# Kernel tuning notes

Hardware: AMD Instinct MI355X
Metric: run time of the kernel (lower is better)

The kernel has to match this reference:

```python
import jax, jax.numpy as jnp
import numpy as np

B, T, D, H = 4, 2048, 1024, 16
DK, DV, K, I = 48, 96, 4, 3072
EPS = 1e-5


def rmsnorm(x, w, eps=EPS):
    return x * jax.lax.rsqrt(jnp.mean(x * x, -1, keepdims=True) + eps) * w


def l2norm(x, eps=1e-6):
    return x * jax.lax.rsqrt(jnp.sum(x * x, -1, keepdims=True) + eps)


def causal_conv(x, w):
    # x: [B,T,C], w: [C,K]; causal depthwise conv (torch cross-correlation semantics)
    k = w.shape[1]
    xp = jnp.pad(x, ((0, 0), (k - 1, 0), (0, 0))).transpose(0, 2, 1)  # [B,C,T+K-1]
    y = jax.lax.conv_general_dilated(xp, w[:, None, :], (1,), 'VALID',
                                     feature_group_count=w.shape[0])
    return y.transpose(0, 2, 1)


def gated_delta_rule(q, k, v, g, beta):
    # q,k: [B,T,H,DK]  v: [B,T,H,DV]  g,beta: [B,T,H]
    scale = q.shape[-1] ** -0.5
    qT = jnp.moveaxis(q, 1, 0) * scale
    kT = jnp.moveaxis(k, 1, 0)
    vT = jnp.moveaxis(v, 1, 0)
    gT = jnp.moveaxis(g, 1, 0)
    bT = jnp.moveaxis(beta, 1, 0)
    S0 = jnp.zeros((q.shape[0], q.shape[2], q.shape[3], v.shape[3]), q.dtype)

    def step(S, inp):
        q_t, k_t, v_t, g_t, b_t = inp
        S = S * jnp.exp(g_t)[..., None, None]                      # gated decay
        v_new = (v_t - jnp.einsum('bhk,bhkv->bhv', k_t, S)) * b_t[..., None]
        S = S + k_t[..., None] * v_new[..., None, :]               # delta-rule update
        o_t = jnp.einsum('bhk,bhkv->bhv', q_t, S)
        return S, o_t

    _, o = jax.lax.scan(step, S0, (qT, kT, vT, gT, bT))
    return jnp.moveaxis(o, 0, 1)


def setup_inputs() -> dict:
    key = jax.random.key(0)
    ks = jax.random.split(key, 20)
    s = 0.02
    return {
        'hidden_states': jax.random.normal(ks[0], (B, T, D), jnp.float32),
        'norm1_w': jnp.ones((D,), jnp.float32),
        'q_w': jax.random.normal(ks[1], (D, H * DK), jnp.float32) * s,
        'k_w': jax.random.normal(ks[2], (D, H * DK), jnp.float32) * s,
        'v_w': jax.random.normal(ks[3], (D, H * DV), jnp.float32) * s,
        'conv_q_w': jax.random.normal(ks[4], (H * DK, K), jnp.float32) * 0.2,
        'conv_k_w': jax.random.normal(ks[5], (H * DK, K), jnp.float32) * 0.2,
        'conv_v_w': jax.random.normal(ks[6], (H * DV, K), jnp.float32) * 0.2,
        'b_w': jax.random.normal(ks[7], (D, H), jnp.float32) * s,
        'a_w': jax.random.normal(ks[8], (D, H), jnp.float32) * s,
        'A_log': jnp.log(jax.random.uniform(ks[9], (H,), jnp.float32, 1.0, 16.0)),
        'dt_bias': jax.random.normal(ks[10], (H,), jnp.float32) * 0.5,
        'g_w': jax.random.normal(ks[11], (D, H * DV), jnp.float32) * s,
        'o_norm_w': jnp.ones((DV,), jnp.float32),
        'o_w': jax.random.normal(ks[12], (H * DV, D), jnp.float32) * s,
        'norm2_w': jnp.ones((D,), jnp.float32),
        'gate_w': jax.random.normal(ks[13], (D, I), jnp.float32) * s,
        'up_w': jax.random.normal(ks[14], (D, I), jnp.float32) * s,
        'down_w': jax.random.normal(ks[15], (I, D), jnp.float32) * s,
    }


def reference(hidden_states, norm1_w, q_w, k_w, v_w, conv_q_w, conv_k_w, conv_v_w,
              b_w, a_w, A_log, dt_bias, g_w, o_norm_w, o_w, norm2_w,
              gate_w, up_w, down_w):
    x = hidden_states
    h = rmsnorm(x, norm1_w)
    # --- GatedDeltaNet mixer ---
    q = jax.nn.silu(causal_conv(h @ q_w, conv_q_w)).reshape(B, T, H, DK)
    k = jax.nn.silu(causal_conv(h @ k_w, conv_k_w)).reshape(B, T, H, DK)
    v = jax.nn.silu(causal_conv(h @ v_w, conv_v_w)).reshape(B, T, H, DV)
    q, k = l2norm(q), l2norm(k)
    beta = jax.nn.sigmoid(h @ b_w)                                  # [B,T,H]
    g = -jnp.exp(A_log) * jax.nn.softplus(h @ a_w + dt_bias)        # [B,T,H] mamba gate
    o = gated_delta_rule(q, k, v, g, beta)                          # [B,T,H,DV]
    gate = (h @ g_w).reshape(B, T, H, DV)
    o = rmsnorm(o, o_norm_w) * (gate * jax.nn.sigmoid(gate))        # fused gated RMSNorm
    x = x + o.reshape(B, T, H * DV) @ o_w
    # --- SwiGLU MLP ---
    h2 = rmsnorm(x, norm2_w)
    x = x + (jax.nn.silu(h2 @ gate_w) * (h2 @ up_w)) @ down_w
    return x
```

## Files before the change

kernel.cpp:

```cpp
#include <hip/hip_runtime.h>
#include <hip/hip_bf16.h>
#include <math.h>

constexpr int Bn = 4, Tn = 2048, Dn = 1024, Hn = 16, DKn = 48, DVn = 96, In = 3072;
constexpr int BT = Bn * Tn;
constexpr int HDK = Hn * DKn;
constexpr int HDV = Hn * DVn;
constexpr int QKVC = 2 * HDK + HDV;
constexpr int CC = 64;
constexpr int NC = Tn / CC;

using bf16 = __hip_bfloat16;
typedef __attribute__((ext_vector_type(8))) short bf16x8;
typedef __attribute__((ext_vector_type(4))) float f32x4;

constexpr size_t WO_HBF   = 0;
constexpr size_t WO_QKVR  = 16777216;
constexpr size_t WO_OSC   = 16777216;
constexpr size_t WO_ATTN  = 41943040;
constexpr size_t WO_ACT   = 16777216;
constexpr size_t WO_A     = 16777216;
constexpr size_t WO_B     = 26214400;
constexpr size_t WO_ST    = 45088768;
constexpr size_t WO_QKVC  = 67108864;
constexpr size_t WO_GATE  = 117440512;
constexpr size_t WO_X1    = 142606336;
constexpr size_t WO_BA    = 176160768;
constexpr size_t WO_GC    = 177209344;
constexpr size_t WO_T     = 177733632;
constexpr size_t WO_UV    = 194510848;
constexpr size_t WO_WB    = 219676672;
constexpr size_t WB_QKVT = 0;
constexpr size_t WB_GT   = 3145728;
constexpr size_t WB_OT   = 4718592;
constexpr size_t WB_GATET= 6291456;
constexpr size_t WB_UPT  = 9437184;
constexpr size_t WB_DOWNT= 12582912;
constexpr size_t WB_ABT  = 15728640;

__device__ __forceinline__ float sigmoidf_(float x) { return 1.f / (1.f + __expf(-x)); }
__device__ __forceinline__ float siluf(float x) { return x * sigmoidf_(x); }

__device__ __forceinline__ void glds16(const void* g, void* l) {
  __builtin_amdgcn_global_load_lds((const __attribute__((address_space(1))) void*)g,
                                   (__attribute__((address_space(3))) void*)l, 16, 0, 0);
}

__device__ __forceinline__ f32x4 mfma16(bf16x8 a, bf16x8 b, f32x4 c) {
  return __builtin_amdgcn_mfma_f32_16x16x32_bf16(a, b, c, 0, 0, 0);
}

__device__ __forceinline__ bf16x8 scale8(bf16x8 a, float s) {
  bf16x8 r;
#pragma unroll
  for (int e = 0; e < 8; e++) {
    float f = __bfloat162float(__ushort_as_bfloat16((unsigned short)a[e])) * s;
    r[e] = (short)__bfloat16_as_ushort(__float2bfloat16(f));
  }
  return r;
}

__device__ __forceinline__ float b2f(short u) {
  return __bfloat162float(__ushort_as_bfloat16((unsigned short)u));
}
__device__ __forceinline__ short f2b(float f) {
  return (short)__bfloat16_as_ushort(__float2bfloat16(f));
}

struct TcastArgs {
  const float* src[10];
  bf16* dst[10];
  int R[10], C[10], gxw[10], t0[10];
};

__global__ void tcast_all(TcastArgs a) {
  __shared__ float t[32][33];
  int bid = blockIdx.x;
  int i = 0;
#pragma unroll
  for (int k = 1; k < 10; k++) if (bid >= a.t0[k]) i = k;
  int lt = bid - a.t0[i];
  int gxw = a.gxw[i];
  int bx = lt % gxw, by = lt / gxw;
  const float* in = a.src[i];
  bf16* out = a.dst[i];
  int R = a.R[i], C = a.C[i];
  int tx = threadIdx.x, ty = threadIdx.y;
  int c0 = bx * 32, r0 = by * 32;
#pragma unroll
  for (int j = 0; j < 4; j++) {
    int r = ty + j * 8;
    float v = (c0 + tx < C) ? in[(size_t)(r0 + r) * C + c0 + tx] : 0.f;
    t[r][tx] = v;
  }
  __syncthreads();
#pragma unroll
  for (int j = 0; j < 4; j++) {
    int cc = ty + j * 8;
    if (c0 + cc < C) out[(size_t)(c0 + cc) * R + r0 + tx] = __float2bfloat16(t[tx][cc]);
  }
}

__global__ void rmsnorm_bf_k(const float* __restrict__ x, const float* __restrict__ w,
                             bf16* __restrict__ y) {
  int row = blockIdx.x;
  const float4* xr = (const float4*)(x + (size_t)row * Dn);
  int tid = threadIdx.x;
  float4 v = xr[tid];
  float ss = v.x * v.x + v.y * v.y + v.z * v.z + v.w * v.w;
  for (int m = 32; m >= 1; m >>= 1) ss += __shfl_xor(ss, m, 64);
  __shared__ float wsum[4];
  if ((tid & 63) == 0) wsum[tid >> 6] = ss;
  __syncthreads();
  ss = wsum[0] + wsum[1] + wsum[2] + wsum[3];
  float rs = rsqrtf(ss * (1.f / Dn) + 1e-5f);
  float4 wv = ((const float4*)w)[tid];
  bf16* yr = y + (size_t)row * Dn + tid * 4;
  yr[0] = __float2bfloat16(v.x * rs * wv.x);
  yr[1] = __float2bfloat16(v.y * rs * wv.y);
  yr[2] = __float2bfloat16(v.z * rs * wv.z);
  yr[3] = __float2bfloat16(v.w * rs * wv.w);
}

#define AS256(bi) (lds + (bi) * 8192)
#define BS256(bi) (lds + 32768 + (bi) * 8192)
#define STAGE256(bi, k0) do { \
    glds16(gA0 + (k0), AS256(bi) + w * 512); \
    glds16(gA1 + (k0), AS256(bi) + 4096 + w * 512); \
    glds16(gB0 + (k0), BS256(bi) + w * 512); \
    glds16(gB1 + (k0), BS256(bi) + 4096 + w * 512); \
  } while (0)

__global__ __launch_bounds__(512, 2) void gemm256(
    const bf16* __restrict__ A, const bf16* __restrict__ Bt,
    bf16* __restrict__ C0, bf16* __restrict__ C1,
    int gx, int N, int K, int mode) {
  __shared__ bf16 lds[65536];
  int nb = gx * 32;
  int q8 = nb >> 3;
  int bid = blockIdx.x;
  int sw = (bid & 7) * q8 + (bid >> 3);
  int by = sw & 31, bx = sw >> 5;
  int bm = by * 256, bn = bx * 256;
  int tid = threadIdx.x;
  int lane = tid & 63, w = tid >> 6;
  int l15 = lane & 15, lq = lane >> 4;
  int wr = w >> 2, wc = w & 3;
  int arow0 = tid >> 2;
  int srcq = (tid & 3) ^ ((arow0 >> 1) & 3);
  const bf16* gA0 = A + (size_t)(bm + arow0) * K + srcq * 8;
  const bf16* gA1 = A + (size_t)(bm + 128 + arow0) * K + srcq * 8;
  const bf16* gB0 = Bt + (size_t)(bn + arow0) * K + srcq * 8;
  const bf16* gB1 = Bt + (size_t)(bn + 128 + arow0) * K + srcq * 8;
  int slot = lq ^ ((l15 >> 1) & 3);
  f32x4 acc[8][4];
#pragma unroll
  for (int m = 0; m < 8; m++)
#pragma unroll
    for (int n = 0; n < 4; n++) acc[m][n] = (f32x4){0.f, 0.f, 0.f, 0.f};
  int NT = K >> 5;
  STAGE256(0, 0);
  STAGE256(1, 32);
  STAGE256(2, 64);
  for (int t = 0; t < NT; ++t) {
    int b = t & 3;
    if (t <= NT - 3)      { asm volatile("s_waitcnt vmcnt(8)" ::: "memory"); }
    else if (t == NT - 2) { asm volatile("s_waitcnt vmcnt(4)" ::: "memory"); }
    else                  { asm volatile("s_waitcnt vmcnt(0)" ::: "memory"); }
    __builtin_amdgcn_s_barrier();
    bf16x8 af[8], bfr[4];
#pragma unroll
    for (int m = 0; m < 8; m++)
      af[m] = *(const bf16x8*)(AS256(b) + (wr * 128 + m * 16 + l15) * 32 + slot * 8);
#pragma unroll
    for (int n = 0; n < 4; n++)
      bfr[n] = *(const bf16x8*)(BS256(b) + (wc * 64 + n * 16 + l15) * 32 + slot * 8);
    __builtin_amdgcn_s_setprio(1);
#pragma unroll
    for (int m = 0; m < 8; m++)
#pragma unroll
      for (int n = 0; n < 4; n++)
        acc[m][n] = mfma16(af[m], bfr[n], acc[m][n]);
    __builtin_amdgcn_s_setprio(0);
    if (t + 3 < NT) STAGE256((t + 3) & 3, (t + 3) * 32);
  }
  __syncthreads();
  bf16* dst; int ldc, bnl; bool doSilu;
  if (mode == 10) {
    if (bn < 3072) { dst = C0; ldc = 3072; bnl = bn; doSilu = false; }
    else           { dst = C1; ldc = 1536; bnl = bn - 3072; doSilu = false; }
  } else {
    if (bn < 3072) { dst = C0; ldc = 3072; bnl = bn; doSilu = true; }
    else           { dst = C1; ldc = 3072; bnl = bn - 3072; doSilu = false; }
  }
  bf16* cw = lds + w * 8192;
#pragma unroll
  for (int m = 0; m < 8; m++)
#pragma unroll
    for (int n = 0; n < 4; n++)
#pragma unroll
      for (int i = 0; i < 4; i++) {
        int row_l = m * 16 + lq * 4 + i;
        int col_l = n * 16 + l15;
        float v = acc[m][n][i];
        if (doSilu) v = siluf(v);
        cw[row_l * 64 + col_l] = __float2bfloat16(v);
      }
  __syncthreads();
  int r8 = lane >> 3, c8 = (lane & 7) * 8;
#pragma unroll
  for (int it = 0; it < 16; it++) {
    int row_l = it * 8 + r8;
    bf16x8 val = *(const bf16x8*)&cw[row_l * 64 + c8];
    *(bf16x8*)&dst[(size_t)(bm + wr * 128 + row_l) * ldc + bnl + wc * 64 + c8] = val;
  }
}

#define STAGE128(bi, k0) do { \
    { int c0_ = 2 * w4; \
      int arow_ = bm + c0_ * 16 + srow; \
      glds16(A + (size_t)arow_ * K + (k0) + gq * 8, &As[bi][c0_ * 512]); \
      int brow_ = bn + c0_ * 16 + srow; if (brow_ >= N) brow_ = 0; \
      glds16(Bt + (size_t)brow_ * K + (k0) + gq * 8, &Bs[bi][c0_ * 512]); \
      int c1_ = c0_ + 1; \
      int arow2_ = bm + c1_ * 16 + srow; \
      glds16(A + (size_t)arow2_ * K + (k0) + gq * 8, &As[bi][c1_ * 512]); \
      int brow2_ = bn + c1_ * 16 + srow; if (brow2_ >= N) brow2_ = 0; \
      glds16(Bt + (size_t)brow2_ * K + (k0) + gq * 8, &Bs[bi][c1_ * 512]); \
    } \
  } while (0)

__global__ __launch_bounds__(256) void gemm_mfma(
    const bf16* __restrict__ A, const bf16* __restrict__ Bt,
    void* __restrict__ Cv, const float* __restrict__ res,
    int N, int K, int ldc, int mode) {
  __shared__ bf16 As[4][4096];
  __shared__ bf16 Bs[4][4096];
  int tid = threadIdx.x, lane = tid & 63, w4 = tid >> 6;
  int bm = blockIdx.y * 128, bn = blockIdx.x * 128;
  int wr = w4 >> 1, wc = w4 & 1;
  int srow = lane >> 2;
  int gq = (lane & 3) ^ ((lane >> 3) & 3);
  int qa = (lane >> 4) ^ ((lane >> 1) & 3);
  int arow_base = wr * 64 + (lane & 15);
  int brow_base = wc * 64 + (lane & 15);
  f32x4 acc[4][4];
#pragma unroll
  for (int m = 0; m < 4; m++)
#pragma unroll
    for (int n = 0; n < 4; n++) acc[m][n] = (f32x4){0.f, 0.f, 0.f, 0.f};
  int NT = K >> 5;
  STAGE128(0, 0);
  STAGE128(1, 32);
  STAGE128(2, 64);
  for (int t = 0; t < NT; ++t) {
    int b = t & 3;
    if (t <= NT - 3)      { asm volatile("s_waitcnt vmcnt(8)" ::: "memory"); }
    else if (t == NT - 2) { asm volatile("s_waitcnt vmcnt(4)" ::: "memory"); }
    else                  { asm volatile("s_waitcnt vmcnt(0)" ::: "memory"); }
    __builtin_amdgcn_s_barrier();
    bf16x8 af[4], bfr[4];
#pragma unroll
    for (int m = 0; m < 4; m++)
      af[m] = *(const bf16x8*)&As[b][(arow_base + m * 16) * 32 + qa * 8];
#pragma unroll
    for (int n = 0; n < 4; n++)
      bfr[n] = *(const bf16x8*)&Bs[b][(brow_base + n * 16) * 32 + qa * 8];
    __builtin_amdgcn_s_setprio(1);
#pragma unroll
    for (int m = 0; m < 4; m++)
#pragma unroll
      for (int n = 0; n < 4; n++)
        acc[m][n] = mfma16(af[m], bfr[n], acc[m][n]);
    __builtin_amdgcn_s_setprio(0);
    if (t + 3 < NT) STAGE128((t + 3) & 3, (t + 3) * 32);
  }
#pragma unroll
  for (int m = 0; m < 4; m++) {
#pragma unroll
    for (int n = 0; n < 4; n++) {
      int col = bn + wc * 64 + n * 16 + (lane & 15);
      if (col >= N) continue;
#pragma unroll
      for (int i = 0; i < 4; i++) {
        int row = bm + wr * 64 + m * 16 + (lane >> 4) * 4 + i;
        float v = acc[m][n][i];
        size_t idx = (size_t)row * ldc + col;
        if (mode == 0) {
          if (res) v += res[idx];
          ((float*)Cv)[idx] = v;
        } else {
          ((bf16*)Cv)[idx] = __float2bfloat16(v);
        }
      }
    }
  }
}

__global__ __launch_bounds__(256) void convsilu2_k(const bf16* __restrict__ in,
                                                   bf16* __restrict__ outp,
                                                   const float* __restrict__ wq,
                                                   const float* __restrict__ wk,
                                                   const float* __restrict__ wv) {
  int tx = threadIdx.x & 31;
  int ty = threadIdx.x >> 5;
  int c = (blockIdx.x * 32 + tx) * 8;
  int gt = blockIdx.y * 8 + ty;
  int b = gt >> 11, t = gt & (Tn - 1);
  const float* wsrc = (c < HDK) ? (wq + c * 4)
                     : (c < 2 * HDK) ? (wk + (c - HDK) * 4)
                                     : (wv + (c - 2 * HDK) * 4);
  float4 W[8];
#pragma unroll
  for (int j = 0; j < 8; j++) W[j] = ((const float4*)wsrc)[j];
  const bf16* base = in + (size_t)b * Tn * QKVC + c;
  bf16x8 r[4];
  bf16x8 zero = {0, 0, 0, 0, 0, 0, 0, 0};
#pragma unroll
  for (int j = 0; j < 4; j++) {
    int tt = t - 3 + j;
    r[j] = (tt >= 0) ? *(const bf16x8*)(base + (size_t)tt * QKVC) : zero;
  }
  bf16x8 o;
#pragma unroll
  for (int ch = 0; ch < 8; ch++) {
    float x0 = b2f(r[0][ch]), x1 = b2f(r[1][ch]), x2 = b2f(r[2][ch]), x3 = b2f(r[3][ch]);
    float y = x0 * W[ch].x + x1 * W[ch].y + x2 * W[ch].z + x3 * W[ch].w;
    o[ch] = f2b(siluf(y));
  }
  *(bf16x8*)(outp + (size_t)gt * QKVC + c) = o;
}

__global__ __launch_bounds__(256) void l2norm_k(bf16* __restrict__ qkv) {
  int row = blockIdx.x * 256 + threadIdx.x;
  int t = row >> 5, hr = row & 31;
  bf16* p = qkv + (size_t)t * QKVC + hr * DKn;
  bf16x8 v[6];
  float ss = 0.f;
#pragma unroll
  for (int j = 0; j < 6; j++) {
    v[j] = *(const bf16x8*)(p + j * 8);
#pragma unroll
    for (int e = 0; e < 8; e++) { float f = b2f(v[j][e]); ss += f * f; }
  }
  float rs = rsqrtf(ss + 1e-6f);
#pragma unroll
  for (int j = 0; j < 6; j++) {
    bf16x8 o;
#pragma unroll
    for (int e = 0; e < 8; e++) o[e] = f2b(b2f(v[j][e]) * rs);
    *(bf16x8*)(p + j * 8) = o;
  }
}

__global__ void betag_k(float* __restrict__ ba, const float* __restrict__ A_log,
                        const float* __restrict__ dt_bias) {
  int i = blockIdx.x * blockDim.x + threadIdx.x;
  int h = i & 15, r = i >> 4;
  float bv = ba[(size_t)r * 32 + h];
  float av = ba[(size_t)r * 32 + 16 + h];
  ba[(size_t)r * 32 + h] = sigmoidf_(bv);
  float xx = av + dt_bias[h];
  float sp = (xx > 20.f) ? xx : log1pf(__expf(xx));
  ba[(size_t)r * 32 + 16 + h] = -__expf(A_log[h]) * sp;
}

__global__ __launch_bounds__(256) void dn_p1(const bf16* __restrict__ qkv,
                                             const float* __restrict__ ba,
                                             float* __restrict__ Gc_g,
                                             bf16* __restrict__ T_g,
                                             bf16* __restrict__ Uv_g) {
  __shared__ bf16 Kl[64][72];
  __shared__ bf16 Vl[64][100];
  __shared__ float Nl[64][68];
  __shared__ float Gcl[64], Bl[64];
  int cid = blockIdx.x;
  int nc = cid & (NC - 1);
  int bh = cid >> 5;
  int h = bh & 15, b = bh >> 4;
  int t0 = nc * CC;
  int tid = threadIdx.x, lane = tid & 63, w = tid >> 6;
  {
    int t = tid >> 2, p = tid & 3;
    const bf16* row = qkv + ((size_t)(b * Tn + t0 + t)) * QKVC;
    int c0 = p * 12;
#pragma unroll
    for (int j = 0; j < 12; ++j) Kl[t][c0 + j] = row[HDK + h * DKn + c0 + j];
    int j0 = p * 24;
#pragma unroll
    for (int j = 0; j < 24; ++j) Vl[t][j0 + j] = row[2 * HDK + h * DVn + j0 + j];
  }
  for (int i = tid; i < 64 * 24; i += 256) {
    int t = i / 24, c = 48 + (i % 24);
    Kl[t][c] = __float2bfloat16(0.f);
  }
  if (tid < 64) {
    size_t row = (size_t)(b * Tn + t0 + tid);
    float g = ba[row * 32 + 16 + h];
    float be = ba[row * 32 + h];
    float acc = g;
#pragma unroll
    for (int d = 1; d < 64; d <<= 1) {
      float o = __shfl_up(acc, d);
      if (tid >= d) acc += o;
    }
    Gcl[tid] = acc; Bl[tid] = be;
    Gc_g[(size_t)bh * Tn + t0 + tid] = acc;
  }
  __syncthreads();
  f32x4 dacc[4];
#pragma unroll
  for (int n = 0; n < 4; n++) dacc[n] = (f32x4){0.f, 0.f, 0.f, 0.f};
  {
    int arow = w * 16 + (lane & 15);
    int qd = lane >> 4;
    bf16x8 a0 = *(const bf16x8*)&Kl[arow][qd * 8];
    bf16x8 a1 = *(const bf16x8*)&Kl[arow][32 + qd * 8];
#pragma unroll
    for (int n = 0; n < 4; n++) {
      int brow = n * 16 + (lane & 15);
      bf16x8 b0 = *(const bf16x8*)&Kl[brow][qd * 8];
      bf16x8 b1 = *(const bf16x8*)&Kl[brow][32 + qd * 8];
      dacc[n] = mfma16(a0, b0, dacc[n]);
      dacc[n] = mfma16(a1, b1, dacc[n]);
    }
  }
#pragma unroll
  for (int i = 0; i < 4; i++) {
    int t = w * 16 + (lane >> 4) * 4 + i;
    float bt = Bl[t], gt = Gcl[t];
#pragma unroll
    for (int n = 0; n < 4; n++) {
      int s = n * 16 + (lane & 15);
      Nl[t][s] = (s < t) ? bt * __expf(gt - Gcl[s]) * dacc[n][i] : 0.f;
    }
  }
  __syncthreads();
  int c = tid;
  if (c < 160) {
    float R[64];
    if (c < 64) {
#pragma unroll
      for (int t = 0; t < 64; ++t) R[t] = (t == c) ? 1.f : 0.f;
    } else {
      int j = c - 64;
#pragma unroll
      for (int t = 0; t < 64; ++t) R[t] = Bl[t] * __bfloat162float(Vl[t][j]);
    }
#pragma unroll
    for (int t = 1; t < 64; ++t) {
      float a0 = 0.f, a1 = 0.f, a2 = 0.f, a3 = 0.f;
#pragma unroll
      for (int s = 0; s + 3 < t; s += 4) {
        float4 n4 = *(const float4*)&Nl[t][s];
        a0 += n4.x * R[s]; a1 += n4.y * R[s + 1];
        a2 += n4.z * R[s + 2]; a3 += n4.w * R[s + 3];
      }
#pragma unroll
      for (int s = t & ~3; s < t; ++s) a0 += Nl[t][s] * R[s];
      R[t] -= ((a0 + a1) + (a2 + a3));
    }
    if (c < 64) {
#pragma unroll
      for (int t = 0; t < 64; ++t)
        T_g[(size_t)cid * 4096 + t * 64 + c] = __float2bfloat16(R[t]);
    } else {
      int j = c - 64;
#pragma unroll
      for (int t = 0; t < 64; ++t)
        Uv_g[(size_t)cid * 6144 + t * 96 + j] = __float2bfloat16(R[t]);
    }
  }
}

__global__ __launch_bounds__(256) void dn_p2a(const bf16* __restrict__ qkv,
                                              const float* __restrict__ ba,
                                              const float* __restrict__ Gc_g,
                                              const bf16* __restrict__ T_g,
                                              const bf16* __restrict__ Uv_g,
                                              bf16* __restrict__ A_g,
                                              bf16* __restrict__ B_g) {
  __shared__ bf16 Kl[64][72];
  __shared__ bf16 KTl[48][72];
  __shared__ bf16 KTbl[48][72];
  __shared__ bf16 Tl[64][72];
  __shared__ bf16 M2T[48][72];
  __shared__ bf16 UvdT[96][72];
  __shared__ float Gcl[64], Bl[64];
  int cid = blockIdx.x;
  int nc = cid & (NC - 1);
  int bh = cid >> 5;
  int h = bh & 15, b = bh >> 4;
  int t0 = nc * CC;
  int tid = threadIdx.x, lane = tid & 63, w = tid >> 6;
  int l15 = lane & 15, qd = lane >> 4;
  {
    int t = tid >> 2, p = tid & 3;
    const bf16* row = qkv + ((size_t)(b * Tn + t0 + t)) * QKVC;
    int c0 = p * 12;
#pragma unroll
    for (int j = 0; j < 12; ++j) Kl[t][c0 + j] = row[HDK + h * DKn + c0 + j];
  }
  if (tid < 64) {
    size_t row = (size_t)(b * Tn + t0 + tid);
    Gcl[tid] = Gc_g[(size_t)bh * Tn + t0 + tid];
    Bl[tid] = ba[row * 32 + h];
  }
  for (int i = tid; i < 4096; i += 256)
    (&Tl[0][0])[(i >> 6) * 72 + (i & 63)] = T_g[(size_t)cid * 4096 + i];
  unsigned short uvr[24];
#pragma unroll
  for (int r = 0; r < 24; r++)
    uvr[r] = __bfloat16_as_ushort(Uv_g[(size_t)cid * 6144 + tid + 256 * r]);
  __syncthreads();
  float g63 = Gcl[63];
  for (int i = tid; i < 48 * 64; i += 256) {
    int dk = i >> 6, t = i & 63;
    bf16 kv = Kl[t][dk];
    KTl[dk][t] = kv;
    float bl = Bl[t] * __expf(Gcl[t]);
    KTbl[dk][t] = __float2bfloat16(__bfloat162float(kv) * bl);
  }
#pragma unroll
  for (int r = 0; r < 24; r++) {
    int i = tid + 256 * r;
    int t = i / 96, dv = i % 96;
    float dd = __expf(g63 - Gcl[t]);
    UvdT[dv][t] = __float2bfloat16(
        __bfloat162float(__ushort_as_bfloat16(uvr[r])) * dd);
  }
  __syncthreads();
  f32x4 m1[3];
#pragma unroll
  for (int n = 0; n < 3; n++) m1[n] = (f32x4){0.f, 0.f, 0.f, 0.f};
  {
    int arow = w * 16 + l15;
    bf16x8 a0 = *(const bf16x8*)&Tl[arow][qd * 8];
    bf16x8 a1 = *(const bf16x8*)&Tl[arow][32 + qd * 8];
#pragma unroll
    for (int n = 0; n < 3; n++) {
      int brow = n * 16 + l15;
      bf16x8 b0 = *(const bf16x8*)&KTbl[brow][qd * 8];
      bf16x8 b1 = *(const bf16x8*)&KTbl[brow][32 + qd * 8];
      m1[n] = mfma16(a0, b0, m1[n]);
      m1[n] = mfma16(a1, b1, m1[n]);
    }
  }
#pragma unroll
  for (int i = 0; i < 4; i++) {
    int tt = w * 16 + qd * 4 + i;
    float dd = __expf(g63 - Gcl[tt]);
#pragma unroll
    for (int n = 0; n < 3; n++) {
      int dk = n * 16 + l15;
      M2T[dk][tt] = __float2bfloat16(m1[n][i] * dd);
    }
  }
  __syncthreads();
  float lamC = __expf(g63);
#pragma unroll
  for (int tswap = 0; tswap < 7; tswap++) {
    int t = w + 4 * tswap;
    if (t >= 27) break;
    int mi, ni; bool isA;
    if (t < 9) { isA = true; mi = t / 3; ni = t % 3; }
    else { isA = false; mi = (t - 9) / 6; ni = (t - 9) % 6; }
    f32x4 acc = (f32x4){0.f, 0.f, 0.f, 0.f};
    int arow = mi * 16 + l15;
    bf16x8 a0 = *(const bf16x8*)&KTl[arow][qd * 8];
    bf16x8 a1 = *(const bf16x8*)&KTl[arow][32 + qd * 8];
    int brow = ni * 16 + l15;
    if (isA) {
      bf16x8 b0 = *(const bf16x8*)&M2T[brow][qd * 8];
      bf16x8 b1 = *(const bf16x8*)&M2T[brow][32 + qd * 8];
      acc = mfma16(a0, b0, acc);
      acc = mfma16(a1, b1, acc);
#pragma unroll
      for (int i = 0; i < 4; i++) {
        int row = mi * 16 + qd * 4 + i, colv = ni * 16 + l15;
        float v = ((row == colv) ? lamC : 0.f) - acc[i];
        A_g[(size_t)cid * 2304 + row * 48 + colv] = __float2bfloat16(v);
      }
    } else {
      bf16x8 b0 = *(const bf16x8*)&UvdT[brow][qd * 8];
      bf16x8 b1 = *(const bf16x8*)&UvdT[brow][32 + qd * 8];
      acc = mfma16(a0, b0, acc);
      acc = mfma16(a1, b1, acc);
#pragma unroll
      for (int i = 0; i < 4; i++) {
        int row = mi * 16 + qd * 4 + i, colv = ni * 16 + l15;
        B_g[(size_t)cid * 4608 + row * 96 + colv] = __float2bfloat16(acc[i]);
      }
    }
  }
}

__global__ __launch_bounds__(256) void dn_p2b(const bf16* __restrict__ A_g,
                                              const bf16* __restrict__ B_g,
                                              bf16* __restrict__ St_g) {
  __shared__ bf16 STl[2][96][72];
  __shared__ bf16 Al[2][48][72];
  __shared__ bf16 Bl[2][4608];
  int bh = blockIdx.x;
  int tid = threadIdx.x, lane = tid & 63, w = tid >> 6;
  int l15 = lane & 15, qd = lane >> 4;
  bf16 zb = __float2bfloat16(0.f);
  for (int i = tid; i < 2 * 96 * 72; i += 256) (&STl[0][0][0])[i] = zb;
  for (int i = tid; i < 2 * 48 * 24; i += 256) {
    int buf = i / (48 * 24), r = (i / 24) % 48, cc = 48 + (i % 24);
    Al[buf][r][cc] = zb;
  }
  bf16x8 ra0, ra1, rb0, rb1;
  unsigned int rb2;
  int e_a0 = tid * 8, e_a1 = 2048 + tid * 8;
  {
    size_t cid = (size_t)bh * NC;
    ra0 = *(const bf16x8*)(A_g + cid * 2304 + e_a0);
    if (tid < 32) ra1 = *(const bf16x8*)(A_g + cid * 2304 + e_a1);
    rb0 = *(const bf16x8*)(B_g + cid * 4608 + tid * 16);
    rb1 = *(const bf16x8*)(B_g + cid * 4608 + tid * 16 + 8);
    rb2 = *(const unsigned int*)(B_g + cid * 4608 + 4096 + tid * 2);
  }
  *(bf16x8*)&Al[0][e_a0 / 48][e_a0 % 48] = ra0;
  if (tid < 32) *(bf16x8*)&Al[0][e_a1 / 48][e_a1 % 48] = ra1;
  *(bf16x8*)&Bl[0][tid * 16] = rb0;
  *(bf16x8*)&Bl[0][tid * 16 + 8] = rb1;
  *(unsigned int*)&Bl[0][4096 + tid * 2] = rb2;
  {
    size_t cid = (size_t)bh * NC + 1;
    ra0 = *(const bf16x8*)(A_g + cid * 2304 + e_a0);
    if (tid < 32) ra1 = *(const bf16x8*)(A_g + cid * 2304 + e_a1);
    rb0 = *(const bf16x8*)(B_g + cid * 4608 + tid * 16);
    rb1 = *(const bf16x8*)(B_g + cid * 4608 + tid * 16 + 8);
    rb2 = *(const unsigned int*)(B_g + cid * 4608 + 4096 + tid * 2);
  }
  __syncthreads();

  for (int c = 0; c < NC - 1; ++c) {
    int cur = c & 1, nxt = cur ^ 1;
    size_t cid = (size_t)bh * NC + c;
    {
      int e0 = tid * 8, e1 = 2048 + tid * 8, e2 = 4096 + tid * 2;
      *(bf16x8*)(St_g + cid * 4608 + e0) = *(const bf16x8*)&STl[cur][e0 / 48][e0 % 48];
      *(bf16x8*)(St_g + cid * 4608 + e1) = *(const bf16x8*)&STl[cur][e1 / 48][e1 % 48];
      *(unsigned int*)(St_g + cid * 4608 + e2) = *(const unsigned int*)&STl[cur][e2 / 48][e2 % 48];
    }
    float vals[5][4];
#pragma unroll
    for (int ts = 0; ts < 5; ts++) {
      int t = w + 4 * ts;
      if (t >= 18) break;
      int mi = t / 3, ni = t % 3;
      f32x4 acc = (f32x4){0.f, 0.f, 0.f, 0.f};
      int arow = mi * 16 + l15;
      bf16x8 a0 = *(const bf16x8*)&STl[cur][arow][qd * 8];
      bf16x8 a1 = *(const bf16x8*)&STl[cur][arow][32 + qd * 8];
      int brow = ni * 16 + l15;
      bf16x8 b0 = *(const bf16x8*)&Al[cur][brow][qd * 8];
      bf16x8 b1 = *(const bf16x8*)&Al[cur][brow][32 + qd * 8];
      acc = mfma16(a0, b0, acc);
      acc = mfma16(a1, b1, acc);
#pragma unroll
      for (int i = 0; i < 4; i++) {
        int dv = mi * 16 + qd * 4 + i, ii = ni * 16 + l15;
        vals[ts][i] = acc[i] + __bfloat162float(Bl[cur][ii * 96 + dv]);
      }
    }
#pragma unroll
    for (int ts = 0; ts < 5; ts++) {
      int t = w + 4 * ts;
      if (t >= 18) break;
      int mi = t / 3, ni = t % 3;
#pragma unroll
      for (int i = 0; i < 4; i++) {
        int dv = mi * 16 + qd * 4 + i, ii = ni * 16 + l15;
        STl[nxt][dv][ii] = __float2bfloat16(vals[ts][i]);
      }
    }
    if (c + 1 <= NC - 2) {
      *(bf16x8*)&Al[nxt][e_a0 / 48][e_a0 % 48] = ra0;
      if (tid < 32) *(bf16x8*)&Al[nxt][e_a1 / 48][e_a1 % 48] = ra1;
      *(bf16x8*)&Bl[nxt][tid * 16] = rb0;
      *(bf16x8*)&Bl[nxt][tid * 16 + 8] = rb1;
      *(unsigned int*)&Bl[nxt][4096 + tid * 2] = rb2;
      if (c + 2 <= NC - 2) {
        size_t cid2 = (size_t)bh * NC + c + 2;
        ra0 = *(const bf16x8*)(A_g + cid2 * 2304 + e_a0);
        if (tid < 32) ra1 = *(const bf16x8*)(A_g + cid2 * 2304 + e_a1);
        rb0 = *(const bf16x8*)(B_g + cid2 * 4608 + tid * 16);
        rb1 = *(const bf16x8*)(B_g + cid2 * 4608 + tid * 16 + 8);
        rb2 = *(const unsigned int*)(B_g + cid2 * 4608 + 4096 + tid * 2);
      }
    }
    __syncthreads();
  }
  {
    size_t cid = (size_t)bh * NC + (NC - 1);
    int cur = (NC - 1) & 1;
    int e0 = tid * 8, e1 = 2048 + tid * 8, e2 = 4096 + tid * 2;
    *(bf16x8*)(St_g + cid * 4608 + e0) = *(const bf16x8*)&STl[cur][e0 / 48][e0 % 48];
    *(bf16x8*)(St_g + cid * 4608 + e1) = *(const bf16x8*)&STl[cur][e1 / 48][e1 % 48];
    *(unsigned int*)(St_g + cid * 4608 + e2) = *(const unsigned int*)&STl[cur][e2 / 48][e2 % 48];
  }
}

__global__ __launch_bounds__(256) void dn_p2c(const bf16* __restrict__ qkv,
                                              const float* __restrict__ ba,
                                              const float* __restrict__ Gc_g,
                                              const bf16* __restrict__ T_g,
                                              const bf16* __restrict__ Uv_g,
                                              const bf16* __restrict__ St_g,
                                              bf16* __restrict__ osc) {
  __shared__ bf16 Kl[64][72], Ql[64][72], Tl[64][72], Ml[64][72];
  __shared__ bf16 G1T[96][72], UT[96][72], STb[96][72];
  __shared__ float Gcl[64], Bl[64];
  int cid = blockIdx.x;
  int nc = cid & (NC - 1);
  int bh = cid >> 5;
  int h = bh & 15, b = bh >> 4;
  int t0 = nc * CC;
  int tid = threadIdx.x, lane = tid & 63, w = tid >> 6;
  int l15 = lane & 15, qd = lane >> 4;
  const float scale = 0.14433756729740643f;
  bf16 zb = __float2bfloat16(0.f);
  {
    int t = tid >> 2, p = tid & 3;
    size_t grow = (size_t)(b * Tn + t0 + t);
    const bf16* row = qkv + grow * QKVC;
    int c0 = p * 12;
#pragma unroll
    for (int j = 0; j < 12; ++j) {
      int cc = c0 + j;
      Kl[t][cc] = row[HDK + h * DKn + cc];
      Ql[t][cc] = __float2bfloat16(__bfloat162float(row[h * DKn + cc]) * scale);
    }
    if (p == 0) { Gcl[t] = Gc_g[(size_t)bh * Tn + t0 + t]; Bl[t] = ba[grow * 32 + h]; }
  }
  for (int i = tid; i < 64 * 16; i += 256) {
    int t = i >> 4, cc = 48 + (i & 15);
    Kl[t][cc] = zb; Ql[t][cc] = zb;
  }
  for (int i = tid; i < 4096; i += 256)
    (&Tl[0][0])[(i >> 6) * 72 + (i & 63)] = T_g[(size_t)cid * 4096 + i];
  for (int i = tid; i < 4608; i += 256)
    STb[i / 48][i % 48] = St_g[(size_t)cid * 4608 + i];
  for (int i = tid; i < 96 * 16; i += 256)
    STb[i >> 4][48 + (i & 15)] = zb;
  __syncthreads();
  f32x4 acc[6];
#pragma unroll
  for (int n = 0; n < 6; n++) acc[n] = (f32x4){0.f, 0.f, 0.f, 0.f};
  {
    int arow = w * 16 + l15;
    bf16x8 a0 = *(const bf16x8*)&Kl[arow][qd * 8];
    bf16x8 a1 = *(const bf16x8*)&Kl[arow][32 + qd * 8];
#pragma unroll
    for (int n = 0; n < 6; n++) {
      int brow = n * 16 + l15;
      bf16x8 b0 = *(const bf16x8*)&STb[brow][qd * 8];
      bf16x8 b1 = *(const bf16x8*)&STb[brow][32 + qd * 8];
      acc[n] = mfma16(a0, b0, acc[n]);
      acc[n] = mfma16(a1, b1, acc[n]);
    }
  }
#pragma unroll
  for (int i = 0; i < 4; i++) {
    int tt = w * 16 + qd * 4 + i;
    float sc = Bl[tt] * __expf(Gcl[tt]);
#pragma unroll
    for (int n = 0; n < 6; n++)
      G1T[n * 16 + l15][tt] = __float2bfloat16(acc[n][i] * sc);
  }
  __syncthreads();
#pragma unroll
  for (int n = 0; n < 6; n++) acc[n] = (f32x4){0.f, 0.f, 0.f, 0.f};
  {
    int arow = w * 16 + l15;
    bf16x8 a0 = *(const bf16x8*)&Tl[arow][qd * 8];
    bf16x8 a1 = *(const bf16x8*)&Tl[arow][32 + qd * 8];
#pragma unroll
    for (int n = 0; n < 6; n++) {
      int brow = n * 16 + l15;
      bf16x8 b0 = *(const bf16x8*)&G1T[brow][qd * 8];
      bf16x8 b1 = *(const bf16x8*)&G1T[brow][32 + qd * 8];
      acc[n] = mfma16(a0, b0, acc[n]);
      acc[n] = mfma16(a1, b1, acc[n]);
    }
  }
#pragma unroll
  for (int i = 0; i < 4; i++) {
    int tt = w * 16 + qd * 4 + i;
#pragma unroll
    for (int n = 0; n < 6; n++) {
      int dv = n * 16 + l15;
      float uv = __bfloat162float(Uv_g[(size_t)cid * 6144 + tt * 96 + dv]);
      UT[dv][tt] = __float2bfloat16(uv - acc[n][i]);
    }
  }
  f32x4 qk[4];
#pragma unroll
  for (int n = 0; n < 4; n++) qk[n] = (f32x4){0.f, 0.f, 0.f, 0.f};
  {
    int arow = w * 16 + l15;
    bf16x8 a0 = *(const bf16x8*)&Ql[arow][qd * 8];
    bf16x8 a1 = *(const bf16x8*)&Ql[arow][32 + qd * 8];
#pragma unroll
    for (int n = 0; n < 4; n++) {
      int brow = n * 16 + l15;
      bf16x8 b0 = *(const bf16x8*)&Kl[brow][qd * 8];
      bf16x8 b1 = *(const bf16x8*)&Kl[brow][32 + qd * 8];
      qk[n] = mfma16(a0, b0, qk[n]);
      qk[n] = mfma16(a1, b1, qk[n]);
    }
  }
#pragma unroll
  for (int i = 0; i < 4; i++) {
    int tt = w * 16 + qd * 4 + i;
    float gt = Gcl[tt];
#pragma unroll
    for (int n = 0; n < 4; n++) {
      int ss = n * 16 + l15;
      float m = (ss <= tt) ? qk[n][i] * __expf(gt - Gcl[ss]) : 0.f;
      Ml[tt][ss] = __float2bfloat16(m);
    }
  }
  __syncthreads();
#pragma unroll
  for (int n = 0; n < 6; n++) acc[n] = (f32x4){0.f, 0.f, 0.f, 0.f};
  {
    int arow = w * 16 + l15;
    float lam = __expf(Gcl[arow]);
    bf16x8 a0 = scale8(*(const bf16x8*)&Ql[arow][qd * 8], lam);
    bf16x8 a1 = scale8(*(const bf16x8*)&Ql[arow][32 + qd * 8], lam);
    bf16x8 m0 = *(const bf16x8*)&Ml[arow][qd * 8];
    bf16x8 m1 = *(const bf16x8*)&Ml[arow][32 + qd * 8];
#pragma unroll
    for (int n = 0; n < 6; n++) {
      int brow = n * 16 + l15;
      bf16x8 b0 = *(const bf16x8*)&STb[brow][qd * 8];
      bf16x8 b1 = *(const bf16x8*)&STb[brow][32 + qd * 8];
      acc[n] = mfma16(a0, b0, acc[n]);
      acc[n] = mfma16(a1, b1, acc[n]);
      bf16x8 u0 = *(const bf16x8*)&UT[brow][qd * 8];
      bf16x8 u1 = *(const bf16x8*)&UT[brow][32 + qd * 8];
      acc[n] = mfma16(m0, u0, acc[n]);
      acc[n] = mfma16(m1, u1, acc[n]);
    }
  }
#pragma unroll
  for (int i = 0; i < 4; i++) {
    int tt = w * 16 + qd * 4 + i;
    size_t orow = ((size_t)(b * Tn + t0 + tt)) * HDV + h * DVn;
#pragma unroll
    for (int n = 0; n < 6; n++)
      osc[orow + n * 16 + l15] = __float2bfloat16(acc[n][i]);
  }
}

__global__ __launch_bounds__(256) void gatednorm_bf_k(const bf16* __restrict__ o,
                                                      const bf16* __restrict__ gate,
                                                      const float* __restrict__ onw,
                                                      bf16* __restrict__ attn) {
  int row = blockIdx.x * 256 + threadIdx.x;
  const bf16* orow = o + (size_t)row * DVn;
  const bf16* grow = gate + (size_t)row * DVn;
  bf16* arow = attn + (size_t)row * DVn;
  bf16x8 ov[12];
  float ss = 0.f;
#pragma unroll
  for (int j = 0; j < 12; j++) {
    ov[j] = *(const bf16x8*)(orow + j * 8);
#pragma unroll
    for (int e = 0; e < 8; e++) { float f = b2f(ov[j][e]); ss += f * f; }
  }
  float rs = rsqrtf(ss * (1.f / DVn) + 1e-5f);
#pragma unroll
  for (int j = 0; j < 12; j++) {
    bf16x8 gv = *(const bf16x8*)(grow + j * 8);
    bf16x8 av;
#pragma unroll
    for (int e = 0; e < 8; e++) {
      float g = b2f(gv[e]);
      av[e] = f2b(b2f(ov[j][e]) * rs * onw[j * 8 + e] * siluf(g));
    }
    *(bf16x8*)(arow + j * 8) = av;
  }
}

__global__ __launch_bounds__(256) void silumul_bf_k(bf16* __restrict__ a,
                                                    const bf16* __restrict__ b) {
  size_t i = ((size_t)blockIdx.x * 256 + threadIdx.x) * 8;
  bf16x8 av = *(const bf16x8*)(a + i);
  bf16x8 bv = *(const bf16x8*)(b + i);
  bf16x8 r;
#pragma unroll
  for (int e = 0; e < 8; e++) r[e] = f2b(b2f(av[e]) * b2f(bv[e]));
  *(bf16x8*)(a + i) = r;
}

extern "C" void kernel_launch(void* const* d_in, const int* in_sizes, int n_in,
                              void* d_out, int out_size, void* d_ws, size_t ws_size,
                              hipStream_t stream) {
  const float* x       = (const float*)d_in[0];
  const float* norm1_w = (const float*)d_in[1];
  const float* q_w     = (const float*)d_in[2];
  const float* k_w     = (const float*)d_in[3];
  const float* v_w     = (const float*)d_in[4];
  const float* cq_w    = (const float*)d_in[5];
  const float* ck_w    = (const float*)d_in[6];
  const float* cv_w    = (const float*)d_in[7];
  const float* b_w     = (const float*)d_in[8];
  const float* a_w     = (const float*)d_in[9];
  const float* A_log   = (const float*)d_in[10];
  const float* dt_bias = (const float*)d_in[11];
  const float* g_w     = (const float*)d_in[12];
  const float* o_norm_w= (const float*)d_in[13];
  const float* o_w     = (const float*)d_in[14];
  const float* norm2_w = (const float*)d_in[15];
  const float* gate_w  = (const float*)d_in[16];
  const float* up_w    = (const float*)d_in[17];
  const float* down_w  = (const float*)d_in[18];
  char* wsb = (char*)d_ws;
  float* out = (float*)d_out;

  bf16*  hbf   = (bf16*)(wsb + WO_HBF);
  bf16*  qkvr  = (bf16*)(wsb + WO_QKVR);
  bf16*  qkvc  = (bf16*)(wsb + WO_QKVC);
  bf16*  upb   = (bf16*)(wsb + WO_QKVC);
  bf16*  oscb  = (bf16*)(wsb + WO_OSC);
  bf16*  attn  = (bf16*)(wsb + WO_ATTN);
  bf16*  actb  = (bf16*)(wsb + WO_ACT);
  bf16*  gateb = (bf16*)(wsb + WO_GATE);
  float* x1    = (float*)(wsb + WO_X1);
  float* ba    = (float*)(wsb + WO_BA);
  float* Gc    = (float*)(wsb + WO_GC);
  bf16*  Tg    = (bf16*)(wsb + WO_T);
  bf16*  Uvg   = (bf16*)(wsb + WO_UV);
  bf16*  A_g   = (bf16*)(wsb + WO_A);
  bf16*  B_g   = (bf16*)(wsb + WO_B);
  bf16*  St_g  = (bf16*)(wsb + WO_ST);
  bf16*  wb    = (bf16*)(wsb + WO_WB);

  {
    TcastArgs ta;
    const float* srcs[10] = {q_w, k_w, v_w, g_w, o_w, gate_w, up_w, down_w, b_w, a_w};
    bf16* dsts[10] = {wb + WB_QKVT, wb + WB_QKVT + 768 * 1024, wb + WB_QKVT + 1536 * 1024,
                      wb + WB_GT, wb + WB_OT, wb + WB_GATET, wb + WB_UPT, wb + WB_DOWNT,
                      wb + WB_ABT, wb + WB_ABT + 16 * 1024};
    int Rs[10] = {1024, 1024, 1024, 1024, 1536, 1024, 1024, 3072, 1024, 1024};
    int Cs[10] = {768, 768, 1536, 1536, 1024, 3072, 3072, 1024, 16, 16};
    int off = 0;
    for (int i = 0; i < 10; i++) {
      ta.src[i] = srcs[i]; ta.dst[i] = dsts[i];
      ta.R[i] = Rs[i]; ta.C[i] = Cs[i];
      ta.gxw[i] = (Cs[i] + 31) / 32;
      ta.t0[i] = off;
      off += ta.gxw[i] * (Rs[i] / 32);
    }
    tcast_all<<<off, dim3(32, 8), 0, stream>>>(ta);
  }

  rmsnorm_bf_k<<<BT, 256, 0, stream>>>(x, norm1_w, hbf);
  gemm256<<<576, 512, 0, stream>>>(hbf, wb + WB_QKVT, qkvr, gateb, 18, 4608, 1024, 10);
  gemm_mfma<<<dim3(1, 64), 256, 0, stream>>>(hbf, wb + WB_ABT, ba, nullptr, 32, 1024, 32, 0);
  convsilu2_k<<<dim3(QKVC / 256, BT / 8), 256, 0, stream>>>(qkvr, qkvc, cq_w, ck_w, cv_w);
  l2norm_k<<<(BT * 32) / 256, 256, 0, stream>>>(qkvc);
  betag_k<<<(BT * Hn) / 256, 256, 0, stream>>>(ba, A_log, dt_bias);
  dn_p1<<<Bn * Hn * NC, 256, 0, stream>>>(qkvc, ba, Gc, Tg, Uvg);
  dn_p2a<<<Bn * Hn * NC, 256, 0, stream>>>(qkvc, ba, Gc, Tg, Uvg, A_g, B_g);
  dn_p2b<<<Bn * Hn, 256, 0, stream>>>(A_g, B_g, St_g);
  dn_p2c<<<Bn * Hn * NC, 256, 0, stream>>>(qkvc, ba, Gc, Tg, Uvg, St_g, oscb);
  gatednorm_bf_k<<<(BT * Hn) / 256, 256, 0, stream>>>(oscb, gateb, o_norm_w, attn);
  gemm_mfma<<<dim3(8, 64), 256, 0, stream>>>(attn, wb + WB_OT, x1, x, 1024, 1536, 1024, 0);
  rmsnorm_bf_k<<<BT, 256, 0, stream>>>(x1, norm2_w, hbf);
  gemm256<<<768, 512, 0, stream>>>(hbf, wb + WB_GATET, actb, upb, 24, 6144, 1024, 11);
  silumul_bf_k<<<(BT * In) / (8 * 256), 256, 0, stream>>>(actb, upb);
  gemm_mfma<<<dim3(8, 64), 256, 0, stream>>>(actb, wb + WB_DOWNT, out, x1, 1024, 3072, 1024, 0);
}
```

Baseline: 721.6 us.

## Fuse chunk solve into p2a and gated RMSNorm into p2c epilogue

Merges the dn_p1 triangular-solve kernel with dn_p2a, so T and the decayed Uv are written straight into shared memory instead of being read back from global memory. Shared memory is aliased to fit both phases in one block. The gated RMSNorm is also folded into the dn_p2c epilogue using wave shuffles, which removes the separate gatednorm kernel and the intermediate output buffer. The cost is higher shared-memory use per block, which may lower occupancy, plus extra serial work per block.

Measured after the change: 715.0 us. No clear change (-0.9%).

```diff
diff --git a/kernel.cpp b/kernel.cpp
--- a/kernel.cpp
+++ b/kernel.cpp
@@ -17,7 +17,6 @@
 constexpr size_t WO_HBF   = 0;
 constexpr size_t WO_QKVR  = 16777216;
 constexpr size_t WO_OSC   = 16777216;
-constexpr size_t WO_ATTN  = 41943040;
 constexpr size_t WO_ACT   = 16777216;
 constexpr size_t WO_A     = 16777216;
 constexpr size_t WO_B     = 26214400;
@@ -365,128 +364,24 @@
   ba[(size_t)r * 32 + 16 + h] = -__expf(A_log[h]) * sp;
 }
 
-__global__ __launch_bounds__(256) void dn_p1(const bf16* __restrict__ qkv,
-                                             const float* __restrict__ ba,
-                                             float* __restrict__ Gc_g,
-                                             bf16* __restrict__ T_g,
-                                             bf16* __restrict__ Uv_g) {
-  __shared__ bf16 Kl[64][72];
-  __shared__ bf16 Vl[64][100];
-  __shared__ float Nl[64][68];
-  __shared__ float Gcl[64], Bl[64];
-  int cid = blockIdx.x;
-  int nc = cid & (NC - 1);
-  int bh = cid >> 5;
-  int h = bh & 15, b = bh >> 4;
-  int t0 = nc * CC;
-  int tid = threadIdx.x, lane = tid & 63, w = tid >> 6;
-  {
-    int t = tid >> 2, p = tid & 3;
-    const bf16* row = qkv + ((size_t)(b * Tn + t0 + t)) * QKVC;
-    int c0 = p * 12;
-#pragma unroll
-    for (int j = 0; j < 12; ++j) Kl[t][c0 + j] = row[HDK + h * DKn + c0 + j];
-    int j0 = p * 24;
-#pragma unroll
-    for (int j = 0; j < 24; ++j) Vl[t][j0 + j] = row[2 * HDK + h * DVn + j0 + j];
-  }
-  for (int i = tid; i < 64 * 24; i += 256) {
-    int t = i / 24, c = 48 + (i % 24);
-    Kl[t][c] = __float2bfloat16(0.f);
-  }
-  if (tid < 64) {
-    size_t row = (size_t)(b * Tn + t0 + tid);
-    float g = ba[row * 32 + 16 + h];
-    float be = ba[row * 32 + h];
-    float acc = g;
-#pragma unroll
-    for (int d = 1; d < 64; d <<= 1) {
-      float o = __shfl_up(acc, d);
-      if (tid >= d) acc += o;
-    }
-    Gcl[tid] = acc; Bl[tid] = be;
-    Gc_g[(size_t)bh * Tn + t0 + tid] = acc;
-  }
-  __syncthreads();
-  f32x4 dacc[4];
-#pragma unroll
-  for (int n = 0; n < 4; n++) dacc[n] = (f32x4){0.f, 0.f, 0.f, 0.f};
-  {
-    int arow = w * 16 + (lane & 15);
-    int qd = lane >> 4;
-    bf16x8 a0 = *(const bf16x8*)&Kl[arow][qd * 8];
-    bf16x8 a1 = *(const bf16x8*)&Kl[arow][32 + qd * 8];
-#pragma unroll
-    for (int n = 0; n < 4; n++) {
-      int brow = n * 16 + (lane & 15);
-      bf16x8 b0 = *(const bf16x8*)&Kl[brow][qd * 8];
-      bf16x8 b1 = *(const bf16x8*)&Kl[brow][32 + qd * 8];
-      dacc[n] = mfma16(a0, b0, dacc[n]);
-      dacc[n] = mfma16(a1, b1, dacc[n]);
-    }
-  }
-#pragma unroll
-  for (int i = 0; i < 4; i++) {
-    int t = w * 16 + (lane >> 4) * 4 + i;
-    float bt = Bl[t], gt = Gcl[t];
-#pragma unroll
-    for (int n = 0; n < 4; n++) {
-      int s = n * 16 + (lane & 15);
-      Nl[t][s] = (s < t) ? bt * __expf(gt - Gcl[s]) * dacc[n][i] : 0.f;
-    }
-  }
-  __syncthreads();
-  int c = tid;
-  if (c < 160) {
-    float R[64];
-    if (c < 64) {
-#pragma unroll
-      for (int t = 0; t < 64; ++t) R[t] = (t == c) ? 1.f : 0.f;
-    } else {
-      int j = c - 64;
-#pragma unroll
-      for (int t = 0; t < 64; ++t) R[t] = Bl[t] * __bfloat162float(Vl[t][j]);
-    }
-#pragma unroll
-    for (int t = 1; t < 64; ++t) {
-      float a0 = 0.f, a1 = 0.f, a2 = 0.f, a3 = 0.f;
-#pragma unroll
-      for (int s = 0; s + 3 < t; s += 4) {
-        float4 n4 = *(const float4*)&Nl[t][s];
-        a0 += n4.x * R[s]; a1 += n4.y * R[s + 1];
-        a2 += n4.z * R[s + 2]; a3 += n4.w * R[s + 3];
-      }
-#pragma unroll
-      for (int s = t & ~3; s < t; ++s) a0 += Nl[t][s] * R[s];
-      R[t] -= ((a0 + a1) + (a2 + a3));
-    }
-    if (c < 64) {
-#pragma unroll
-      for (int t = 0; t < 64; ++t)
-        T_g[(size_t)cid * 4096 + t * 64 + c] = __float2bfloat16(R[t]);
-    } else {
-      int j = c - 64;
-#pragma unroll
-      for (int t = 0; t < 64; ++t)
-        Uv_g[(size_t)cid * 6144 + t * 96 + j] = __float2bfloat16(R[t]);
-    }
-  }
-}
-
-__global__ __launch_bounds__(256) void dn_p2a(const bf16* __restrict__ qkv,
+__global__ __launch_bounds__(256) void dn_p1a(const bf16* __restrict__ qkv,
                                               const float* __restrict__ ba,
-                                              const float* __restrict__ Gc_g,
-                                              const bf16* __restrict__ T_g,
-                                              const bf16* __restrict__ Uv_g,
+                                              float* __restrict__ Gc_g,
+                                              bf16* __restrict__ T_g,
+                                              bf16* __restrict__ Uv_g,
                                               bf16* __restrict__ A_g,
                                               bf16* __restrict__ B_g) {
-  __shared__ bf16 Kl[64][72];
-  __shared__ bf16 KTl[48][72];
-  __shared__ bf16 KTbl[48][72];
-  __shared__ bf16 Tl[64][72];
-  __shared__ bf16 M2T[48][72];
-  __shared__ bf16 UvdT[96][72];
-  __shared__ float Gcl[64], Bl[64];
+  __shared__ __align__(16) char smem[62976];
+  bf16 (*Kl)[72]   = (bf16(*)[72])(smem);
+  bf16 (*Tl)[72]   = (bf16(*)[72])(smem + 9216);
+  bf16 (*UvdT)[72] = (bf16(*)[72])(smem + 18432);
+  float* Gcl = (float*)(smem + 32256);
+  float* Bl  = (float*)(smem + 32512);
+  bf16 (*Vl)[100]  = (bf16(*)[100])(smem + 32768);
+  float (*Nl)[68]  = (float(*)[68])(smem + 45568);
+  bf16 (*KTl)[72]  = (bf16(*)[72])(smem + 32768);
+  bf16 (*KTbl)[72] = (bf16(*)[72])(smem + 39680);
+  bf16 (*M2T)[72]  = (bf16(*)[72])(smem + 46592);
   int cid = blockIdx.x;
   int nc = cid & (NC - 1);
   int bh = cid >> 5;
@@ -494,40 +389,110 @@
   int t0 = nc * CC;
   int tid = threadIdx.x, lane = tid & 63, w = tid >> 6;
   int l15 = lane & 15, qd = lane >> 4;
+  bf16 zb = __float2bfloat16(0.f);
   {
     int t = tid >> 2, p = tid & 3;
     const bf16* row = qkv + ((size_t)(b * Tn + t0 + t)) * QKVC;
     int c0 = p * 12;
 #pragma unroll
     for (int j = 0; j < 12; ++j) Kl[t][c0 + j] = row[HDK + h * DKn + c0 + j];
+    int j0 = p * 24;
+#pragma unroll
+    for (int j = 0; j < 24; ++j) Vl[t][j0 + j] = row[2 * HDK + h * DVn + j0 + j];
+  }
+  for (int i = tid; i < 64 * 24; i += 256) {
+    int t = i / 24, c = 48 + (i % 24);
+    Kl[t][c] = zb;
   }
   if (tid < 64) {
     size_t row = (size_t)(b * Tn + t0 + tid);
-    Gcl[tid] = Gc_g[(size_t)bh * Tn + t0 + tid];
-    Bl[tid] = ba[row * 32 + h];
-  }
-  for (int i = tid; i < 4096; i += 256)
-    (&Tl[0][0])[(i >> 6) * 72 + (i & 63)] = T_g[(size_t)cid * 4096 + i];
-  unsigned short uvr[24];
-#pragma unroll
-  for (int r = 0; r < 24; r++)
-    uvr[r] = __bfloat16_as_ushort(Uv_g[(size_t)cid * 6144 + tid + 256 * r]);
+    float g = ba[row * 32 + 16 + h];
+    float be = ba[row * 32 + h];
+    float acc = g;
+#pragma unroll
+    for (int d = 1; d < 64; d <<= 1) {
+      float o = __shfl_up(acc, d);
+      if (tid >= d) acc += o;
+    }
+    Gcl[tid] = acc; Bl[tid] = be;
+    Gc_g[(size_t)bh * Tn + t0 + tid] = acc;
+  }
+  __syncthreads();
+  f32x4 dacc[4];
+#pragma unroll
+  for (int n = 0; n < 4; n++) dacc[n] = (f32x4){0.f, 0.f, 0.f, 0.f};
+  {
+    int arow = w * 16 + l15;
+    bf16x8 a0 = *(const bf16x8*)&Kl[arow][qd * 8];
+    bf16x8 a1 = *(const bf16x8*)&Kl[arow][32 + qd * 8];
+#pragma unroll
+    for (int n = 0; n < 4; n++) {
+      int brow = n * 16 + l15;
+      bf16x8 b0 = *(const bf16x8*)&Kl[brow][qd * 8];
+      bf16x8 b1 = *(const bf16x8*)&Kl[brow][32 + qd * 8];
+      dacc[n] = mfma16(a0, b0, dacc[n]);
+      dacc[n] = mfma16(a1, b1, dacc[n]);
+    }
+  }
+#pragma unroll
+  for (int i = 0; i < 4; i++) {
+    int t = w * 16 + qd * 4 + i;
+    float bt = Bl[t], gt = Gcl[t];
+#pragma unroll
+    for (int n = 0; n < 4; n++) {
+      int s = n * 16 + l15;
+      Nl[t][s] = (s < t) ? bt * __expf(gt - Gcl[s]) * dacc[n][i] : 0.f;
+    }
+  }
   __syncthreads();
   float g63 = Gcl[63];
+  int c = tid;
+  if (c < 160) {
+    float R[64];
+    if (c < 64) {
+#pragma unroll
+      for (int t = 0; t < 64; ++t) R[t] = (t == c) ? 1.f : 0.f;
+    } else {
+      int j = c - 64;
+#pragma unroll
+      for (int t = 0; t < 64; ++t) R[t] = Bl[t] * __bfloat162float(Vl[t][j]);
+    }
+#pragma unroll
+    for (int t = 1; t < 64; ++t) {
+      float a0 = 0.f, a1 = 0.f, a2 = 0.f, a3 = 0.f;
+#pragma unroll
+      for (int s = 0; s + 3 < t; s += 4) {
+        float4 n4 = *(const float4*)&Nl[t][s];
+        a0 += n4.x * R[s]; a1 += n4.y * R[s + 1];
+        a2 += n4.z * R[s + 2]; a3 += n4.w * R[s + 3];
+      }
+#pragma unroll
+      for (int s = t & ~3; s < t; ++s) a0 += Nl[t][s] * R[s];
+      R[t] -= ((a0 + a1) + (a2 + a3));
+    }
+    if (c < 64) {
+#pragma unroll
+      for (int t = 0; t < 64; ++t) {
+        bf16 v = __float2bfloat16(R[t]);
+        T_g[(size_t)cid * 4096 + t * 64 + c] = v;
+        Tl[t][c] = v;
+      }
+    } else {
+      int j = c - 64;
+#pragma unroll
+      for (int t = 0; t < 64; ++t) {
+        Uv_g[(size_t)cid * 6144 + t * 96 + j] = __float2bfloat16(R[t]);
+        UvdT[j][t] = __float2bfloat16(R[t] * __expf(g63 - Gcl[t]));
+      }
+    }
+  }
+  __syncthreads();
   for (int i = tid; i < 48 * 64; i += 256) {
     int dk = i >> 6, t = i & 63;
     bf16 kv = Kl[t][dk];
     KTl[dk][t] = kv;
     float bl = Bl[t] * __expf(Gcl[t]);
     KTbl[dk][t] = __float2bfloat16(__bfloat162float(kv) * bl);
-  }
-#pragma unroll
-  for (int r = 0; r < 24; r++) {
-    int i = tid + 256 * r;
-    int t = i / 96, dv = i % 96;
-    float dd = __expf(g63 - Gcl[t]);
-    UvdT[dv][t] = __float2bfloat16(
-        __bfloat162float(__ushort_as_bfloat16(uvr[r])) * dd);
   }
   __syncthreads();
   f32x4 m1[3];
@@ -710,10 +675,13 @@
                                               const bf16* __restrict__ T_g,
                                               const bf16* __restrict__ Uv_g,
                                               const bf16* __restrict__ St_g,
-                                              bf16* __restrict__ osc) {
+                                              const bf16* __restrict__ gate,
+                                              const float* __restrict__ onw,
+                                              bf16* __restrict__ attn) {
   __shared__ bf16 Kl[64][72], Ql[64][72], Tl[64][72], Ml[64][72];
   __shared__ bf16 G1T[96][72], UT[96][72], STb[96][72];
   __shared__ float Gcl[64], Bl[64];
+  __shared__ float onwl[96];
   int cid = blockIdx.x;
   int nc = cid & (NC - 1);
   int bh = cid >> 5;
@@ -736,6 +704,7 @@
     }
     if (p == 0) { Gcl[t] = Gc_g[(size_t)bh * Tn + t0 + t]; Bl[t] = ba[grow * 32 + h]; }
   }
+  if (tid < 96) onwl[tid] = onw[tid];
   for (int i = tid; i < 64 * 16; i += 256) {
     int t = i >> 4, cc = 48 + (i & 15);
     Kl[t][cc] = zb; Ql[t][cc] = zb;
@@ -850,40 +819,21 @@
 #pragma unroll
   for (int i = 0; i < 4; i++) {
     int tt = w * 16 + qd * 4 + i;
+    float ss = 0.f;
+#pragma unroll
+    for (int n = 0; n < 6; n++) ss += acc[n][i] * acc[n][i];
+    ss += __shfl_xor(ss, 1, 64);
+    ss += __shfl_xor(ss, 2, 64);
+    ss += __shfl_xor(ss, 4, 64);
+    ss += __shfl_xor(ss, 8, 64);
+    float rs = rsqrtf(ss * (1.f / DVn) + 1e-5f);
     size_t orow = ((size_t)(b * Tn + t0 + tt)) * HDV + h * DVn;
 #pragma unroll
-    for (int n = 0; n < 6; n++)
-      osc[orow + n * 16 + l15] = __float2bfloat16(acc[n][i]);
-  }
-}
-
-__global__ __launch_bounds__(256) void gatednorm_bf_k(const bf16* __restrict__ o,
-                                                      const bf16* __restrict__ gate,
-                                                      const float* __restrict__ onw,
-                                                      bf16* __restrict__ attn) {
-  int row = blockIdx.x * 256 + threadIdx.x;
-  const bf16* orow = o + (size_t)row * DVn;
-  const bf16* grow = gate + (size_t)row * DVn;
-  bf16* arow = attn + (size_t)row * DVn;
-  bf16x8 ov[12];
-  float ss = 0.f;
-#pragma unroll
-  for (int j = 0; j < 12; j++) {
-    ov[j] = *(const bf16x8*)(orow + j * 8);
-#pragma unroll
-    for (int e = 0; e < 8; e++) { float f = b2f(ov[j][e]); ss += f * f; }
-  }
-  float rs = rsqrtf(ss * (1.f / DVn) + 1e-5f);
-#pragma unroll
-  for (int j = 0; j < 12; j++) {
-    bf16x8 gv = *(const bf16x8*)(grow + j * 8);
-    bf16x8 av;
-#pragma unroll
-    for (int e = 0; e < 8; e++) {
-      float g = b2f(gv[e]);
-      av[e] = f2b(b2f(ov[j][e]) * rs * onw[j * 8 + e] * siluf(g));
-    }
-    *(bf16x8*)(arow + j * 8) = av;
+    for (int n = 0; n < 6; n++) {
+      int dv = n * 16 + l15;
+      float g = __bfloat162float(gate[orow + dv]);
+      attn[orow + dv] = __float2bfloat16(acc[n][i] * rs * onwl[dv] * siluf(g));
+    }
   }
 }
 
@@ -927,8 +877,7 @@
   bf16*  qkvr  = (bf16*)(wsb + WO_QKVR);
   bf16*  qkvc  = (bf16*)(wsb + WO_QKVC);
   bf16*  upb   = (bf16*)(wsb + WO_QKVC);
-  bf16*  oscb  = (bf16*)(wsb + WO_OSC);
-  bf16*  attn  = (bf16*)(wsb + WO_ATTN);
+  bf16*  attn  = (bf16*)(wsb + WO_OSC);
   bf16*  actb  = (bf16*)(wsb + WO_ACT);
   bf16*  gateb = (bf16*)(wsb + WO_GATE);
   float* x1    = (float*)(wsb + WO_X1);
@@ -966,11 +915,9 @@
   convsilu2_k<<<dim3(QKVC / 256, BT / 8), 256, 0, stream>>>(qkvr, qkvc, cq_w, ck_w, cv_w);
   l2norm_k<<<(BT * 32) / 256, 256, 0, stream>>>(qkvc);
   betag_k<<<(BT * Hn) / 256, 256, 0, stream>>>(ba, A_log, dt_bias);
-  dn_p1<<<Bn * Hn * NC, 256, 0, stream>>>(qkvc, ba, Gc, Tg, Uvg);
-  dn_p2a<<<Bn * Hn * NC, 256, 0, stream>>>(qkvc, ba, Gc, Tg, Uvg, A_g, B_g);
+  dn_p1a<<<Bn * Hn * NC, 256, 0, stream>>>(qkvc, ba, Gc, Tg, Uvg, A_g, B_g);
   dn_p2b<<<Bn * Hn, 256, 0, stream>>>(A_g, B_g, St_g);
-  dn_p2c<<<Bn * Hn * NC, 256, 0, stream>>>(qkvc, ba, Gc, Tg, Uvg, St_g, oscb);
-  gatednorm_bf_k<<<(BT * Hn) / 256, 256, 0, stream>>>(oscb, gateb, o_norm_w, attn);
+  dn_p2c<<<Bn * Hn * NC, 256, 0, stream>>>(qkvc, ba, Gc, Tg, Uvg, St_g, gateb, o_norm_w, attn);
   gemm_mfma<<<dim3(8, 64), 256, 0, stream>>>(attn, wb + WB_OT, x1, x, 1024, 1536, 1024, 0);
   rmsnorm_bf_k<<<BT, 256, 0, stream>>>(x1, norm2_w, hbf);
   gemm256<<<768, 512, 0, stream>>>(hbf, wb + WB_GATET, actb, upb, 24, 6144, 1024, 11);
```
